# Kernel optimization log

Measured on AMD Instinct MI355X. Metric: run time of the kernel, lower is better.

Reference implementation:

```python
import jax, jax.numpy as jnp
import numpy as np

HEADS = 8
DIM_HEAD = 32
SCALE = DIM_HEAD ** -0.5
EPS = 1e-12  # F.normalize eps


def _rmsnorm_ch(t, g):
    # F.normalize(t, dim=1) * g * sqrt(C)  (normalize_dim=1)
    c = t.shape[1]
    norm = jnp.sqrt(jnp.sum(t * t, axis=1, keepdims=True))
    return t / jnp.maximum(norm, EPS) * g[None, :, None, None] * (c ** 0.5)


def setup_inputs() -> dict:
    key = jax.random.key(0)
    ks = jax.random.split(key, 4)
    B, C, H, W = 16, 256, 64, 64
    hidden = HEADS * DIM_HEAD  # 256
    x = jax.random.normal(ks[0], (B, C, H, W), dtype=jnp.float32)
    g1 = jnp.ones((C,), dtype=jnp.float32)
    # conv 1x1 weights stored as [out_ch, in_ch]
    w_qkv = jax.random.normal(ks[1], (hidden * 3, C), dtype=jnp.float32) * (1.0 / np.sqrt(C))
    w_out = jax.random.normal(ks[2], (C, hidden), dtype=jnp.float32) * (1.0 / np.sqrt(hidden))
    b_out = jnp.zeros((C,), dtype=jnp.float32)
    g2 = jnp.ones((C,), dtype=jnp.float32)
    return {"x": x, "g1": g1, "w_qkv": w_qkv, "w_out": w_out, "b_out": b_out, "g2": g2}


def reference(x, g1, w_qkv, w_out, b_out, g2):
    b, c, h, w = x.shape
    n = h * w
    xn = _rmsnorm_ch(x, g1)
    # 1x1 conv (no bias) == channel matmul
    qkv = jnp.einsum('oc,bchw->bohw', w_qkv, xn)
    q, k, v = jnp.split(qkv, 3, axis=1)
    # b (h c) x y -> b h c (x y)
    q = q.reshape(b, HEADS, DIM_HEAD, n)
    k = k.reshape(b, HEADS, DIM_HEAD, n)
    v = v.reshape(b, HEADS, DIM_HEAD, n)
    q = jax.nn.softmax(q, axis=-2) * SCALE  # softmax over dim_head
    k = jax.nn.softmax(k, axis=-1)          # softmax over sequence
    context = jnp.einsum('bhdn,bhen->bhde', k, v)  # [b,h,d,e] small
    out = jnp.einsum('bhde,bhdn->bhen', context, q)
    out = out.reshape(b, HEADS * DIM_HEAD, h, w)
    out = jnp.einsum('oc,bchw->bohw', w_out, out) + b_out[None, :, None, None]
    return _rmsnorm_ch(out, g2) + x
```

## Files before the change

kernel.cpp:

```cpp
#include <hip/hip_runtime.h>
#include <math.h>


#define B_ 16
#define C_ 256
#define N_ 4096
#define SCALE_ 0.17677669529663687f
#define EPS_ 1e-12f

typedef __attribute__((ext_vector_type(8))) short bf16x8;
typedef __attribute__((ext_vector_type(4))) float f32x4;

__device__ __forceinline__ ushort f2bf(float f) {
    union { float f; uint u; } x; x.f = f;
    uint r = (x.u + 0x7FFFu + ((x.u >> 16) & 1u)) >> 16;
    return (ushort)r;
}
__device__ __forceinline__ float bf2f(ushort s) {
    union { uint u; float f; } x; x.u = ((uint)s) << 16;
    return x.f;
}

__global__ __launch_bounds__(256) void k_prep(const float* __restrict__ w_qkv,
                                              const float* __restrict__ g1,
                                              ushort* __restrict__ Wp) {
    int o = blockIdx.x, c = threadIdx.x;
    Wp[(size_t)o * 256 + c] = f2bf(w_qkv[(size_t)o * 256 + c] * g1[c]);
}

__global__ __launch_bounds__(256) void k_xconv(const float* __restrict__ x,
                                               ushort* __restrict__ xnbT) {
    __shared__ float ssp[4][64];
    __shared__ float rinv_s[64];
    __shared__ ushort T[64][268];
    int b = blockIdx.y, n0 = blockIdx.x * 64;
    const float* xb = x + (size_t)b * C_ * N_ + n0;
    int t = threadIdx.x;
    int nl = t & 63, cg = t >> 6;
    float ss = 0.f;
    #pragma unroll 8
    for (int i = 0; i < 64; ++i) {
        float v = xb[(size_t)(cg * 64 + i) * N_ + nl];
        ss += v * v;
    }
    ssp[cg][nl] = ss;
    __syncthreads();
    if (t < 64)
        rinv_s[t] = 16.f / fmaxf(sqrtf(ssp[0][t] + ssp[1][t] + ssp[2][t] + ssp[3][t]), EPS_);
    __syncthreads();
    float rv = rinv_s[nl];
    #pragma unroll 8
    for (int i = 0; i < 64; ++i) {
        int c = cg * 64 + i;
        T[nl][c] = f2bf(xb[(size_t)c * N_ + nl] * rv);
    }
    __syncthreads();
    int j = t >> 2, ch = t & 3;
    ushort* orow = xnbT + ((size_t)b * N_ + n0 + j) * 256 + ch * 64;
    #pragma unroll
    for (int i = 0; i < 8; ++i)
        *(uint2*)&orow[i * 8] = *(const uint2*)&T[j][ch * 64 + i * 8],
        *(uint2*)&orow[i * 8 + 4] = *(const uint2*)&T[j][ch * 64 + i * 8 + 4];
}

__global__ __launch_bounds__(256) void k_gemm(const ushort* __restrict__ Wp,
                                              const ushort* __restrict__ xnbT,
                                              ushort* __restrict__ kvOut) {
    __shared__ ushort Asub[128][40];
    __shared__ ushort Bsub[128][40];
    const int b = blockIdx.z;
    const int wrow0 = 256 + blockIdx.y * 128;
    const int col0 = blockIdx.x * 128;
    const int t = threadIdx.x;
    const int l = t & 63, w = t >> 6;
    const int wr = w >> 1, wc = w & 1, grp = l >> 4;
    const ushort* xb = xnbT + (size_t)b * N_ * 256;
    f32x4 acc[4][4] = {};

    for (int k0 = 0; k0 < 256; k0 += 32) {
        int r = t >> 1, ko = (t & 1) * 16;
        const uint4* sa = (const uint4*)(Wp + (size_t)(wrow0 + r) * 256 + k0 + ko);
        *(uint4*)&Asub[r][ko]     = sa[0];
        *(uint4*)&Asub[r][ko + 8] = sa[1];
        const uint4* sb = (const uint4*)(xb + (size_t)(col0 + r) * 256 + k0 + ko);
        *(uint4*)&Bsub[r][ko]     = sb[0];
        *(uint4*)&Bsub[r][ko + 8] = sb[1];
        __syncthreads();
        bf16x8 af[4], bfv[4];
        #pragma unroll
        for (int m = 0; m < 4; ++m)
            af[m] = *(const bf16x8*)&Asub[wr * 64 + m * 16 + (l & 15)][grp * 8];
        #pragma unroll
        for (int n = 0; n < 4; ++n)
            bfv[n] = *(const bf16x8*)&Bsub[wc * 64 + n * 16 + (l & 15)][grp * 8];
        #pragma unroll
        for (int m = 0; m < 4; ++m)
            #pragma unroll
            for (int n = 0; n < 4; ++n)
                acc[m][n] = __builtin_amdgcn_mfma_f32_16x16x32_bf16(af[m], bfv[n], acc[m][n], 0, 0, 0);
        __syncthreads();
    }

    ushort* kvb = kvOut + (size_t)b * 512 * N_;
    #pragma unroll
    for (int n = 0; n < 4; ++n) {
        int cg = col0 + wc * 64 + n * 16 + (l & 15);
        #pragma unroll
        for (int m = 0; m < 4; ++m) {
            int rbase = wrow0 - 256 + wr * 64 + m * 16 + grp * 4;
            #pragma unroll
            for (int r = 0; r < 4; ++r)
                kvb[(size_t)(rbase + r) * N_ + cg] = f2bf(acc[m][n][r]);
        }
    }
}

__global__ __launch_bounds__(256) void k_ctxpart(const ushort* __restrict__ kv,
                                                 float* __restrict__ ctxp,
                                                 float* __restrict__ sums_p) {
    __shared__ float red[4][32][33];
    __shared__ float redp[4][32];
    int bh = blockIdx.x, s = blockIdx.y;
    int b = bh >> 3, h = bh & 7;
    int t = threadIdx.x, l = t & 63, w = t >> 6;
    const ushort* kb = kv + (size_t)b * 512 * N_ + (size_t)(h * 32) * N_;
    const ushort* vb = kv + (size_t)b * 512 * N_ + (size_t)(256 + h * 32) * N_;
    const int n0base = s * 1024 + w * 256;
    const int row = l & 15, grp = l >> 4;
    f32x4 acc[2][2] = {};
    float psA = 0.f, psB = 0.f;

    for (int it = 0; it < 8; ++it) {
        int n0 = n0base + it * 32 + grp * 8;
        bf16x8 k0 = *(const bf16x8*)&kb[(size_t)row * N_ + n0];
        bf16x8 k1 = *(const bf16x8*)&kb[(size_t)(row + 16) * N_ + n0];
        bf16x8 v0 = *(const bf16x8*)&vb[(size_t)row * N_ + n0];
        bf16x8 v1 = *(const bf16x8*)&vb[(size_t)(row + 16) * N_ + n0];
        bf16x8 p0, p1;
        #pragma unroll
        for (int j = 0; j < 8; ++j) {
            ushort r0 = f2bf(__expf(bf2f((ushort)k0[j])));
            ushort r1 = f2bf(__expf(bf2f((ushort)k1[j])));
            p0[j] = (short)r0; p1[j] = (short)r1;
            psA += bf2f(r0); psB += bf2f(r1);
        }
        acc[0][0] = __builtin_amdgcn_mfma_f32_16x16x32_bf16(p0, v0, acc[0][0], 0, 0, 0);
        acc[0][1] = __builtin_amdgcn_mfma_f32_16x16x32_bf16(p0, v1, acc[0][1], 0, 0, 0);
        acc[1][0] = __builtin_amdgcn_mfma_f32_16x16x32_bf16(p1, v0, acc[1][0], 0, 0, 0);
        acc[1][1] = __builtin_amdgcn_mfma_f32_16x16x32_bf16(p1, v1, acc[1][1], 0, 0, 0);
    }

    psA += __shfl_xor(psA, 16); psA += __shfl_xor(psA, 32);
    psB += __shfl_xor(psB, 16); psB += __shfl_xor(psB, 32);
    #pragma unroll
    for (int mi = 0; mi < 2; ++mi)
        #pragma unroll
        for (int ni = 0; ni < 2; ++ni)
            #pragma unroll
            for (int r = 0; r < 4; ++r)
                red[w][mi * 16 + grp * 4 + r][ni * 16 + row] = acc[mi][ni][r];
    if (l < 16) { redp[w][l] = psA; redp[w][16 + l] = psB; }
    __syncthreads();

    size_t base = (size_t)(s * 128 + bh) * 32;
    #pragma unroll
    for (int i = t; i < 1024; i += 256) {
        int d = i >> 5, e = i & 31;
        ctxp[(base + d) * 32 + e] =
            red[0][d][e] + red[1][d][e] + red[2][d][e] + red[3][d][e];
    }
    if (t < 32)
        sums_p[base + t] = redp[0][t] + redp[1][t] + redp[2][t] + redp[3][t];
}

__global__ __launch_bounds__(256) void k_fold(const float* __restrict__ w_out,
                                              const float* __restrict__ ctxp,
                                              const float* __restrict__ sums_p,
                                              ushort* __restrict__ M) {
    __shared__ float cn[32][33];
    __shared__ float sinv[32];
    int bh = blockIdx.x;
    int b = bh >> 3, h = bh & 7;
    int t = threadIdx.x;
    if (t < 32) {
        float st = 0.f;
        #pragma unroll
        for (int s = 0; s < 4; ++s) st += sums_p[(size_t)(s * 128 + bh) * 32 + t];
        sinv[t] = SCALE_ / st;
    }
    #pragma unroll
    for (int i = t; i < 1024; i += 256) {
        int d = i >> 5, e = i & 31;
        float cv = 0.f;
        #pragma unroll
        for (int s = 0; s < 4; ++s)
            cv += ctxp[((size_t)(s * 128 + bh) * 32 + d) * 32 + e];
        cn[e][d] = cv;
    }
    __syncthreads();
    float wreg[32];
    const float* wr = w_out + (size_t)t * 256 + h * 32;
    #pragma unroll
    for (int e = 0; e < 32; e += 4) {
        float4 wv = *(const float4*)&wr[e];
        wreg[e] = wv.x; wreg[e + 1] = wv.y; wreg[e + 2] = wv.z; wreg[e + 3] = wv.w;
    }
    float acc[32] = {};
    #pragma unroll
    for (int e = 0; e < 32; ++e) {
        float we = wreg[e];
        #pragma unroll
        for (int d = 0; d < 32; ++d) acc[d] += we * cn[e][d];
    }
    ushort* Mrow = M + ((size_t)b * 256 + t) * 256 + h * 32;
    #pragma unroll
    for (int d = 0; d < 32; ++d) Mrow[d] = f2bf(acc[d] * sinv[d]);
}

__global__ __launch_bounds__(512) void k_qfinal(const ushort* __restrict__ Wp,
                                                const ushort* __restrict__ xnbT,
                                                const ushort* __restrict__ M,
                                                const float* __restrict__ b_out,
                                                const float* __restrict__ g2,
                                                const float* __restrict__ x,
                                                float* __restrict__ out) {
    __shared__ ushort BQ[64 * 256];
    __shared__ float ss2[8][64];
    const int b = blockIdx.y, col0 = blockIdx.x * 64;
    const int t = threadIdx.x, l = t & 63, w = t >> 6;
    const int lr = l & 15, grp = l >> 4;
    const ushort* xb = xnbT + (size_t)b * N_ * 256;

    {
        int row = t >> 3, seg = t & 7;
        const uint4* src = (const uint4*)(xb + (size_t)(col0 + row) * 256 + seg * 32);
        uint base = (uint)(row * 512 + seg * 64);
        uint sw = (uint)((row & 7) << 4);
        #pragma unroll
        for (int i = 0; i < 4; ++i)
            *(uint4*)((char*)BQ + ((base + i * 16) ^ sw)) = src[i];
    }
    __syncthreads();

    f32x4 acc[2][4] = {};
    for (int k0 = 0; k0 < 256; k0 += 32) {
        bf16x8 af[2], bf[4];
        #pragma unroll
        for (int m = 0; m < 2; ++m)
            af[m] = *(const bf16x8*)(Wp + (size_t)(w * 32 + m * 16 + lr) * 256 + k0 + grp * 8);
        #pragma unroll
        for (int n = 0; n < 4; ++n) {
            int row = n * 16 + lr;
            uint off = (uint)(row * 512 + (k0 + grp * 8) * 2) ^ (uint)((row & 7) << 4);
            bf[n] = *(const bf16x8*)((const char*)BQ + off);
        }
        #pragma unroll
        for (int m = 0; m < 2; ++m)
            #pragma unroll
            for (int n = 0; n < 4; ++n)
                acc[m][n] = __builtin_amdgcn_mfma_f32_16x16x32_bf16(af[m], bf[n], acc[m][n], 0, 0, 0);
    }
    __syncthreads();

    #pragma unroll
    for (int n = 0; n < 4; ++n) {
        float f[2][4];
        #pragma unroll
        for (int m = 0; m < 2; ++m)
            #pragma unroll
            for (int r = 0; r < 4; ++r) f[m][r] = acc[m][n][r];
        float mx = -1e30f;
        #pragma unroll
        for (int r = 0; r < 4; ++r) mx = fmaxf(mx, fmaxf(f[0][r], f[1][r]));
        mx = fmaxf(mx, __shfl_xor(mx, 16));
        mx = fmaxf(mx, __shfl_xor(mx, 32));
        float s = 0.f;
        #pragma unroll
        for (int r = 0; r < 4; ++r) {
            f[0][r] = __expf(f[0][r] - mx); s += f[0][r];
            f[1][r] = __expf(f[1][r] - mx); s += f[1][r];
        }
        s += __shfl_xor(s, 16); s += __shfl_xor(s, 32);
        float inv = 1.f / s;
        int cl = n * 16 + lr;
        #pragma unroll
        for (int m = 0; m < 2; ++m) {
            int d = w * 32 + m * 16 + grp * 4;
            uint2 pk;
            pk.x = (uint)f2bf(f[m][0] * inv) | ((uint)f2bf(f[m][1] * inv) << 16);
            pk.y = (uint)f2bf(f[m][2] * inv) | ((uint)f2bf(f[m][3] * inv) << 16);
            uint off = (uint)(cl * 512 + d * 2) ^ (uint)((cl & 7) << 4);
            *(uint2*)((char*)BQ + off) = pk;
        }
    }
    __syncthreads();

    f32x4 acc2[2][4] = {};
    const ushort* Mb = M + (size_t)b * 256 * 256;
    for (int k0 = 0; k0 < 256; k0 += 32) {
        bf16x8 af[2], bq[4];
        #pragma unroll
        for (int m = 0; m < 2; ++m)
            af[m] = *(const bf16x8*)(Mb + (size_t)(w * 32 + m * 16 + lr) * 256 + k0 + grp * 8);
        #pragma unroll
        for (int n = 0; n < 4; ++n) {
            int row = n * 16 + lr;
            uint off = (uint)(row * 512 + (k0 + grp * 8) * 2) ^ (uint)((row & 7) << 4);
            bq[n] = *(const bf16x8*)((const char*)BQ + off);
        }
        #pragma unroll
        for (int m = 0; m < 2; ++m)
            #pragma unroll
            for (int n = 0; n < 4; ++n)
                acc2[m][n] = __builtin_amdgcn_mfma_f32_16x16x32_bf16(af[m], bq[n], acc2[m][n], 0, 0, 0);
    }

    #pragma unroll
    for (int n = 0; n < 4; ++n) {
        float local = 0.f;
        #pragma unroll
        for (int m = 0; m < 2; ++m) {
            int obase = w * 32 + m * 16 + grp * 4;
            #pragma unroll
            for (int r = 0; r < 4; ++r) {
                float f = acc2[m][n][r] + b_out[obase + r];
                acc2[m][n][r] = f;
                local += f * f;
            }
        }
        local += __shfl_xor(local, 16);
        local += __shfl_xor(local, 32);
        if (grp == 0) ss2[w][n * 16 + lr] = local;
    }
    __syncthreads();
    const float* xb2 = x + (size_t)b * C_ * N_;
    float* ob = out + (size_t)b * C_ * N_;
    #pragma unroll
    for (int n = 0; n < 4; ++n) {
        int cl = n * 16 + lr;
        int cg = col0 + cl;
        float tot = ss2[0][cl] + ss2[1][cl] + ss2[2][cl] + ss2[3][cl]
                  + ss2[4][cl] + ss2[5][cl] + ss2[6][cl] + ss2[7][cl];
        float rs = 16.f / fmaxf(sqrtf(tot), EPS_);
        #pragma unroll
        for (int m = 0; m < 2; ++m) {
            int obase = w * 32 + m * 16 + grp * 4;
            #pragma unroll
            for (int r = 0; r < 4; ++r) {
                int o = obase + r;
                ob[(size_t)o * N_ + cg] = acc2[m][n][r] * rs * g2[o] + xb2[(size_t)o * N_ + cg];
            }
        }
    }
}

extern "C" void kernel_launch(void* const* d_in, const int* in_sizes, int n_in,
                              void* d_out, int out_size, void* d_ws, size_t ws_size,
                              hipStream_t stream) {
    const float* x     = (const float*)d_in[0];
    const float* g1    = (const float*)d_in[1];
    const float* w_qkv = (const float*)d_in[2];
    const float* w_out = (const float*)d_in[3];
    const float* b_out = (const float*)d_in[4];
    const float* g2    = (const float*)d_in[5];
    float* out = (float*)d_out;
    char* ws = (char*)d_ws;

    ushort* Wp     = (ushort*)(ws + 0);
    float*  ctxp   = (float*)(ws + 393216);
    float*  sums_p = (float*)(ws + 2490368);
    ushort* Mm     = (ushort*)(ws + 2555904);
    ushort* xnbT   = (ushort*)(ws + 4653056);
    ushort* kv     = (ushort*)(ws + 38207488);

    k_prep<<<768, 256, 0, stream>>>(w_qkv, g1, Wp);
    k_xconv<<<dim3(64, 16), 256, 0, stream>>>(x, xnbT);
    k_gemm<<<dim3(32, 4, 16), 256, 0, stream>>>(Wp, xnbT, kv);
    k_ctxpart<<<dim3(128, 4), 256, 0, stream>>>(kv, ctxp, sums_p);
    k_fold<<<128, 256, 0, stream>>>(w_out, ctxp, sums_p, Mm);
    k_qfinal<<<dim3(64, 16), 512, 0, stream>>>(Wp, xnbT, Mm, b_out, g2, x, out);
}
```

Measured before the change: 155.3 us.

## Fuse K/V projection GEMM with context accumulation to drop kv round-trip

Merges the K/V projection GEMM and the per-head context reduction into one kernel. Each block keeps its 128-column tile of the normalized input in swizzled LDS, computes exp(K) and V there, then forms partial context and row sums with MFMA, using a ones-vector MFMA for the sums. This removes writing and re-reading the full bf16 kv tensor through global memory. In exchange it uses about 148KB of dynamic LDS per block, which limits occupancy, and the fold kernel now reduces 32 partials instead of 4.

```diff
diff --git a/kernel.cpp b/kernel.cpp
--- a/kernel.cpp
+++ b/kernel.cpp
@@ -63,114 +63,133 @@
         *(uint2*)&orow[i * 8 + 4] = *(const uint2*)&T[j][ch * 64 + i * 8 + 4];
 }
 
-__global__ __launch_bounds__(256) void k_gemm(const ushort* __restrict__ Wp,
-                                              const ushort* __restrict__ xnbT,
-                                              ushort* __restrict__ kvOut) {
-    __shared__ ushort Asub[128][40];
-    __shared__ ushort Bsub[128][40];
-    const int b = blockIdx.z;
-    const int wrow0 = 256 + blockIdx.y * 128;
-    const int col0 = blockIdx.x * 128;
-    const int t = threadIdx.x;
-    const int l = t & 63, w = t >> 6;
-    const int wr = w >> 1, wc = w & 1, grp = l >> 4;
+__global__ __launch_bounds__(512) void k_kvctx(const ushort* __restrict__ Wp,
+                                               const ushort* __restrict__ xnbT,
+                                               float* __restrict__ ctxp,
+                                               float* __restrict__ sums_p) {
+    extern __shared__ char lds[];
+    ushort (*Asub)[40] = (ushort(*)[40])lds;
+    char* BQ = lds + 20480;
+    char* P  = lds + 86016;
+    const int b = blockIdx.y, s = blockIdx.x;
+    const int col0 = s * 128;
+    const int t = threadIdx.x, l = t & 63, w = t >> 6;
+    const int lr = l & 15, grp = l >> 4;
+    const int wn = w & 3, wo = w >> 2;
     const ushort* xb = xnbT + (size_t)b * N_ * 256;
-    f32x4 acc[4][4] = {};
-
-    for (int k0 = 0; k0 < 256; k0 += 32) {
-        int r = t >> 1, ko = (t & 1) * 16;
-        const uint4* sa = (const uint4*)(Wp + (size_t)(wrow0 + r) * 256 + k0 + ko);
-        *(uint4*)&Asub[r][ko]     = sa[0];
-        *(uint4*)&Asub[r][ko + 8] = sa[1];
-        const uint4* sb = (const uint4*)(xb + (size_t)(col0 + r) * 256 + k0 + ko);
-        *(uint4*)&Bsub[r][ko]     = sb[0];
-        *(uint4*)&Bsub[r][ko + 8] = sb[1];
-        __syncthreads();
-        bf16x8 af[4], bfv[4];
-        #pragma unroll
-        for (int m = 0; m < 4; ++m)
-            af[m] = *(const bf16x8*)&Asub[wr * 64 + m * 16 + (l & 15)][grp * 8];
-        #pragma unroll
-        for (int n = 0; n < 4; ++n)
-            bfv[n] = *(const bf16x8*)&Bsub[wc * 64 + n * 16 + (l & 15)][grp * 8];
-        #pragma unroll
-        for (int m = 0; m < 4; ++m)
-            #pragma unroll
-            for (int n = 0; n < 4; ++n)
-                acc[m][n] = __builtin_amdgcn_mfma_f32_16x16x32_bf16(af[m], bfv[n], acc[m][n], 0, 0, 0);
-        __syncthreads();
-    }
-
-    ushort* kvb = kvOut + (size_t)b * 512 * N_;
-    #pragma unroll
-    for (int n = 0; n < 4; ++n) {
-        int cg = col0 + wc * 64 + n * 16 + (l & 15);
-        #pragma unroll
-        for (int m = 0; m < 4; ++m) {
-            int rbase = wrow0 - 256 + wr * 64 + m * 16 + grp * 4;
+
+    {
+        int row = t >> 2, seg = t & 3;
+        const uint4* src = (const uint4*)(xb + (size_t)(col0 + row) * 256 + seg * 64);
+        uint base = (uint)(row * 512 + seg * 128);
+        uint sw = (uint)((row & 7) << 4);
+        #pragma unroll
+        for (int i = 0; i < 8; ++i)
+            *(uint4*)(BQ + ((base + i * 16) ^ sw)) = src[i];
+    }
+
+    #pragma unroll
+    for (int p = 0; p < 2; ++p) {
+        f32x4 acc[2][8] = {};
+        for (int k0 = 0; k0 < 256; k0 += 32) {
+            {
+                int r = t >> 1, ko = (t & 1) * 16;
+                const uint4* sa = (const uint4*)(Wp + (size_t)(256 + p * 256 + r) * 256 + k0 + ko);
+                *(uint4*)&Asub[r][ko]     = sa[0];
+                *(uint4*)&Asub[r][ko + 8] = sa[1];
+            }
+            __syncthreads();
+            bf16x8 ax[2], bw[8];
+            #pragma unroll
+            for (int m = 0; m < 2; ++m) {
+                int row = wn * 32 + m * 16 + lr;
+                uint off = (uint)(row * 512 + (k0 + grp * 8) * 2) ^ (uint)((row & 7) << 4);
+                ax[m] = *(const bf16x8*)(BQ + off);
+            }
+            #pragma unroll
+            for (int nf = 0; nf < 8; ++nf)
+                bw[nf] = *(const bf16x8*)&Asub[wo * 128 + nf * 16 + lr][grp * 8];
+            #pragma unroll
+            for (int m = 0; m < 2; ++m)
+                #pragma unroll
+                for (int nf = 0; nf < 8; ++nf)
+                    acc[m][nf] = __builtin_amdgcn_mfma_f32_16x16x32_bf16(ax[m], bw[nf], acc[m][nf], 0, 0, 0);
+            __syncthreads();
+        }
+        if (p == 0) {
+            #pragma unroll
+            for (int nf = 0; nf < 8; ++nf) {
+                int d = wo * 128 + nf * 16 + lr;
+                uint sw = (uint)((d & 7) << 4);
+                #pragma unroll
+                for (int m = 0; m < 2; ++m) {
+                    int n0 = wn * 32 + m * 16 + grp * 4;
+                    uint2 pk;
+                    pk.x = (uint)f2bf(__expf(acc[m][nf][0])) | ((uint)f2bf(__expf(acc[m][nf][1])) << 16);
+                    pk.y = (uint)f2bf(__expf(acc[m][nf][2])) | ((uint)f2bf(__expf(acc[m][nf][3])) << 16);
+                    *(uint2*)(P + (((uint)(d * 256 + n0 * 2)) ^ sw)) = pk;
+                }
+            }
+        } else {
+            #pragma unroll
+            for (int nf = 0; nf < 8; ++nf) {
+                int e = wo * 128 + nf * 16 + lr;
+                uint sw = (uint)((e & 7) << 4);
+                #pragma unroll
+                for (int m = 0; m < 2; ++m) {
+                    int n0 = wn * 32 + m * 16 + grp * 4;
+                    uint2 pk;
+                    pk.x = (uint)f2bf(acc[m][nf][0]) | ((uint)f2bf(acc[m][nf][1]) << 16);
+                    pk.y = (uint)f2bf(acc[m][nf][2]) | ((uint)f2bf(acc[m][nf][3]) << 16);
+                    *(uint2*)(BQ + (((uint)(e * 256 + n0 * 2)) ^ sw)) = pk;
+                }
+            }
+        }
+    }
+    __syncthreads();
+
+    const int h = w;
+    f32x4 c3[2][2] = {};
+    f32x4 cS[2] = {};
+    bf16x8 ones;
+    #pragma unroll
+    for (int j = 0; j < 8; ++j) ones[j] = (short)0x3F80;
+    #pragma unroll
+    for (int ks = 0; ks < 4; ++ks) {
+        int n0 = ks * 32 + grp * 8;
+        bf16x8 pA[2], vB[2];
+        #pragma unroll
+        for (int df = 0; df < 2; ++df) {
+            int d = h * 32 + df * 16 + lr;
+            pA[df] = *(const bf16x8*)(P + (((uint)(d * 256 + n0 * 2)) ^ ((uint)((d & 7) << 4))));
+        }
+        #pragma unroll
+        for (int ef = 0; ef < 2; ++ef) {
+            int e = h * 32 + ef * 16 + lr;
+            vB[ef] = *(const bf16x8*)(BQ + (((uint)(e * 256 + n0 * 2)) ^ ((uint)((e & 7) << 4))));
+        }
+        #pragma unroll
+        for (int df = 0; df < 2; ++df) {
+            #pragma unroll
+            for (int ef = 0; ef < 2; ++ef)
+                c3[df][ef] = __builtin_amdgcn_mfma_f32_16x16x32_bf16(pA[df], vB[ef], c3[df][ef], 0, 0, 0);
+            cS[df] = __builtin_amdgcn_mfma_f32_16x16x32_bf16(pA[df], ones, cS[df], 0, 0, 0);
+        }
+    }
+    int bh = b * 8 + h;
+    size_t base = ((size_t)s * 128 + bh) * 32;
+    #pragma unroll
+    for (int df = 0; df < 2; ++df) {
+        #pragma unroll
+        for (int ef = 0; ef < 2; ++ef)
             #pragma unroll
             for (int r = 0; r < 4; ++r)
-                kvb[(size_t)(rbase + r) * N_ + cg] = f2bf(acc[m][n][r]);
-        }
-    }
-}
-
-__global__ __launch_bounds__(256) void k_ctxpart(const ushort* __restrict__ kv,
-                                                 float* __restrict__ ctxp,
-                                                 float* __restrict__ sums_p) {
-    __shared__ float red[4][32][33];
-    __shared__ float redp[4][32];
-    int bh = blockIdx.x, s = blockIdx.y;
-    int b = bh >> 3, h = bh & 7;
-    int t = threadIdx.x, l = t & 63, w = t >> 6;
-    const ushort* kb = kv + (size_t)b * 512 * N_ + (size_t)(h * 32) * N_;
-    const ushort* vb = kv + (size_t)b * 512 * N_ + (size_t)(256 + h * 32) * N_;
-    const int n0base = s * 1024 + w * 256;
-    const int row = l & 15, grp = l >> 4;
-    f32x4 acc[2][2] = {};
-    float psA = 0.f, psB = 0.f;
-
-    for (int it = 0; it < 8; ++it) {
-        int n0 = n0base + it * 32 + grp * 8;
-        bf16x8 k0 = *(const bf16x8*)&kb[(size_t)row * N_ + n0];
-        bf16x8 k1 = *(const bf16x8*)&kb[(size_t)(row + 16) * N_ + n0];
-        bf16x8 v0 = *(const bf16x8*)&vb[(size_t)row * N_ + n0];
-        bf16x8 v1 = *(const bf16x8*)&vb[(size_t)(row + 16) * N_ + n0];
-        bf16x8 p0, p1;
-        #pragma unroll
-        for (int j = 0; j < 8; ++j) {
-            ushort r0 = f2bf(__expf(bf2f((ushort)k0[j])));
-            ushort r1 = f2bf(__expf(bf2f((ushort)k1[j])));
-            p0[j] = (short)r0; p1[j] = (short)r1;
-            psA += bf2f(r0); psB += bf2f(r1);
-        }
-        acc[0][0] = __builtin_amdgcn_mfma_f32_16x16x32_bf16(p0, v0, acc[0][0], 0, 0, 0);
-        acc[0][1] = __builtin_amdgcn_mfma_f32_16x16x32_bf16(p0, v1, acc[0][1], 0, 0, 0);
-        acc[1][0] = __builtin_amdgcn_mfma_f32_16x16x32_bf16(p1, v0, acc[1][0], 0, 0, 0);
-        acc[1][1] = __builtin_amdgcn_mfma_f32_16x16x32_bf16(p1, v1, acc[1][1], 0, 0, 0);
-    }
-
-    psA += __shfl_xor(psA, 16); psA += __shfl_xor(psA, 32);
-    psB += __shfl_xor(psB, 16); psB += __shfl_xor(psB, 32);
-    #pragma unroll
-    for (int mi = 0; mi < 2; ++mi)
-        #pragma unroll
-        for (int ni = 0; ni < 2; ++ni)
+                ctxp[(base + df * 16 + grp * 4 + r) * 32 + ef * 16 + lr] = c3[df][ef][r];
+        if (lr == 0)
             #pragma unroll
             for (int r = 0; r < 4; ++r)
-                red[w][mi * 16 + grp * 4 + r][ni * 16 + row] = acc[mi][ni][r];
-    if (l < 16) { redp[w][l] = psA; redp[w][16 + l] = psB; }
-    __syncthreads();
-
-    size_t base = (size_t)(s * 128 + bh) * 32;
-    #pragma unroll
-    for (int i = t; i < 1024; i += 256) {
-        int d = i >> 5, e = i & 31;
-        ctxp[(base + d) * 32 + e] =
-            red[0][d][e] + red[1][d][e] + red[2][d][e] + red[3][d][e];
-    }
-    if (t < 32)
-        sums_p[base + t] = redp[0][t] + redp[1][t] + redp[2][t] + redp[3][t];
+                sums_p[base + df * 16 + grp * 4 + r] = cS[df][r];
+    }
 }
 
 __global__ __launch_bounds__(256) void k_fold(const float* __restrict__ w_out,
@@ -184,16 +203,16 @@
     int t = threadIdx.x;
     if (t < 32) {
         float st = 0.f;
-        #pragma unroll
-        for (int s = 0; s < 4; ++s) st += sums_p[(size_t)(s * 128 + bh) * 32 + t];
+        #pragma unroll 8
+        for (int s = 0; s < 32; ++s) st += sums_p[(size_t)(s * 128 + bh) * 32 + t];
         sinv[t] = SCALE_ / st;
     }
     #pragma unroll
     for (int i = t; i < 1024; i += 256) {
         int d = i >> 5, e = i & 31;
         float cv = 0.f;
-        #pragma unroll
-        for (int s = 0; s < 4; ++s)
+        #pragma unroll 8
+        for (int s = 0; s < 32; ++s)
             cv += ctxp[((size_t)(s * 128 + bh) * 32 + d) * 32 + e];
         cn[e][d] = cv;
     }
@@ -368,15 +387,16 @@
 
     ushort* Wp     = (ushort*)(ws + 0);
     float*  ctxp   = (float*)(ws + 393216);
-    float*  sums_p = (float*)(ws + 2490368);
-    ushort* Mm     = (ushort*)(ws + 2555904);
-    ushort* xnbT   = (ushort*)(ws + 4653056);
-    ushort* kv     = (ushort*)(ws + 38207488);
+    float*  sums_p = (float*)(ws + 17170432);
+    ushort* Mm     = (ushort*)(ws + 17694720);
+    ushort* xnbT   = (ushort*)(ws + 19791872);
+
+    hipFuncSetAttribute((const void*)k_kvctx,
+                        hipFuncAttributeMaxDynamicSharedMemorySize, 151552);
 
     k_prep<<<768, 256, 0, stream>>>(w_qkv, g1, Wp);
     k_xconv<<<dim3(64, 16), 256, 0, stream>>>(x, xnbT);
-    k_gemm<<<dim3(32, 4, 16), 256, 0, stream>>>(Wp, xnbT, kv);
-    k_ctxpart<<<dim3(128, 4), 256, 0, stream>>>(kv, ctxp, sums_p);
+    k_kvctx<<<dim3(32, 16), 512, 151552, stream>>>(Wp, xnbT, ctxp, sums_p);
     k_fold<<<128, 256, 0, stream>>>(w_out, ctxp, sums_p, Mm);
     k_qfinal<<<dim3(64, 16), 512, 0, stream>>>(Wp, xnbT, Mm, b_out, g2, x, out);
 }
```

New measurement: 146.5 us. 1.06x faster.
